# Performance work log

Hardware: AMD Instinct MI355X
Metric: run time of the kernel (lower is better)

## Reference

```python
import jax, jax.numpy as jnp
import numpy as np

EPS = 1e-05

def setup_inputs() -> dict:
    key = jax.random.key(0)
    k1, k2, k3, k4 = jax.random.split(key, 4)
    B, S, D, K = 32, 1024, 768, 16
    x = jax.random.normal(k1, (B, S, D), dtype=jnp.float32)
    # torch init is ones/zeros, but use nontrivial values for a meaningful check
    weights = jax.random.uniform(k2, (K, D), dtype=jnp.float32)
    biases = jax.random.normal(k3, (K, D), dtype=jnp.float32)
    centroids = jax.random.normal(k4, (K, D), dtype=jnp.float32)
    return {"x": x, "weights": weights, "biases": biases, "centroids": centroids}

def reference(x, weights, biases, centroids):
    # LayerNorm over last dim
    mean = jnp.mean(x, axis=-1, keepdims=True)
    diff = x - mean
    var = jnp.mean(jnp.square(diff), axis=-1, keepdims=True)
    normalized = diff / jnp.sqrt(var + EPS)
    # bucket routing: argmin_k ||x - c_k||_2 ; argmin of squared dist is identical
    x2 = jnp.sum(jnp.square(x), axis=-1, keepdims=True)            # [B,S,1]
    c2 = jnp.sum(jnp.square(centroids), axis=-1)                   # [K]
    xc = jnp.einsum("bsd,kd->bsk", x, centroids)                   # [B,S,K]
    sq_dists = x2 - 2.0 * xc + c2
    selected_buckets = jnp.argmin(sq_dists, axis=-1)               # [B,S] int
    # per-position affine via gather of per-bucket weight/bias
    w = weights[selected_buckets]                                  # [B,S,D]
    b = biases[selected_buckets]                                   # [B,S,D]
    out = normalized * w + b
    return (out, selected_buckets)
```

## Files before the change

### kernel.cpp

```cpp
#include <hip/hip_runtime.h>
#include <math.h>

#define DD 768
#define DD4 192
#define KK 16
#define EPSV 1e-5f
#define SCRS 38

__global__ __launch_bounds__(256, 2)
void sln_kernel(const float* __restrict__ x,
                const float* __restrict__ weights,
                const float* __restrict__ biases,
                const float* __restrict__ centroids,
                float* __restrict__ out,
                float* __restrict__ bkt,
                int nrows)
{
    __shared__ float cs[KK * DD];
    __shared__ float c2s[KK];
    __shared__ float scr[4][16][SCRS];

    const int tid  = threadIdx.x;
    const int lane = tid & 63;
    const int wave = tid >> 6;

    {
        const float4* c4 = (const float4*)centroids;
        float4* cs4w = (float4*)cs;
        for (int i = tid; i < KK * DD4; i += 256) cs4w[i] = c4[i];
    }
    __syncthreads();

    {
        float* part = &scr[0][0][0];
        int k = tid >> 4, t = tid & 15;
        float p = 0.f;
        #pragma unroll
        for (int j = 0; j < DD / 16; ++j) {
            float v = cs[k * DD + t + 16 * j];
            p += v * v;
        }
        part[tid] = p;
    }
    __syncthreads();
    if (tid < KK) {
        float* part = &scr[0][0][0];
        float sacc = 0.f;
        #pragma unroll
        for (int i = 0; i < 16; ++i) sacc += part[tid * 16 + i];
        c2s[tid] = sacc;
    }
    __syncthreads();

    const float4* cs4 = (const float4*)cs;
    const int gw = blockIdx.x * 4 + wave;
    const int wstride = gridDim.x * 4;

    for (int pair = gw; pair * 2 < nrows; pair += wstride) {
        const int r0 = pair * 2;
        const int r1 = r0 + 1;

        const float4* xr0 = (const float4*)(x + (size_t)r0 * DD);
        const float4* xr1 = (const float4*)(x + (size_t)r1 * DD);
        float4 a0 = xr0[lane], a1 = xr0[lane + 64], a2 = xr0[lane + 128];
        float4 b0 = xr1[lane], b1 = xr1[lane + 64], b2 = xr1[lane + 128];

        float s0 = a0.x+a0.y+a0.z+a0.w + a1.x+a1.y+a1.z+a1.w + a2.x+a2.y+a2.z+a2.w;
        float ss0 = a0.x*a0.x+a0.y*a0.y+a0.z*a0.z+a0.w*a0.w
                  + a1.x*a1.x+a1.y*a1.y+a1.z*a1.z+a1.w*a1.w
                  + a2.x*a2.x+a2.y*a2.y+a2.z*a2.z+a2.w*a2.w;
        float s1 = b0.x+b0.y+b0.z+b0.w + b1.x+b1.y+b1.z+b1.w + b2.x+b2.y+b2.z+b2.w;
        float ss1 = b0.x*b0.x+b0.y*b0.y+b0.z*b0.z+b0.w*b0.w
                  + b1.x*b1.x+b1.y*b1.y+b1.z*b1.z+b1.w*b1.w
                  + b2.x*b2.x+b2.y*b2.y+b2.z*b2.z+b2.w*b2.w;

        float d0[KK], d1[KK];
        #pragma unroll
        for (int k = 0; k < KK; ++k) {
            float4 c0 = cs4[k * DD4 + lane];
            float4 c1 = cs4[k * DD4 + lane + 64];
            float4 c2 = cs4[k * DD4 + lane + 128];
            d0[k] = a0.x*c0.x + a0.y*c0.y + a0.z*c0.z + a0.w*c0.w
                  + a1.x*c1.x + a1.y*c1.y + a1.z*c1.z + a1.w*c1.w
                  + a2.x*c2.x + a2.y*c2.y + a2.z*c2.z + a2.w*c2.w;
            d1[k] = b0.x*c0.x + b0.y*c0.y + b0.z*c0.z + b0.w*c0.w
                  + b1.x*c1.x + b1.y*c1.y + b1.z*c1.z + b1.w*c1.w
                  + b2.x*c2.x + b2.y*c2.y + b2.z*c2.z + b2.w*c2.w;
        }

        #pragma unroll
        for (int k = 0; k < KK; ++k) {
            d0[k] += __shfl_xor(d0[k], 1); d0[k] += __shfl_xor(d0[k], 2);
            d1[k] += __shfl_xor(d1[k], 1); d1[k] += __shfl_xor(d1[k], 2);
        }
        s0 += __shfl_xor(s0, 1);  s0 += __shfl_xor(s0, 2);
        ss0 += __shfl_xor(ss0, 1); ss0 += __shfl_xor(ss0, 2);
        s1 += __shfl_xor(s1, 1);  s1 += __shfl_xor(s1, 2);
        ss1 += __shfl_xor(ss1, 1); ss1 += __shfl_xor(ss1, 2);

        if ((lane & 3) == 0) {
            int q = lane >> 2;
            float* p = &scr[wave][q][0];
            #pragma unroll
            for (int k = 0; k < KK; ++k) { p[k] = d0[k]; p[18 + k] = d1[k]; }
            p[16] = s0; p[17] = ss0; p[34] = s1; p[35] = ss1;
        }
        __asm__ volatile("" ::: "memory");

        int slot = (lane < 32) ? lane : (18 + (lane - 32));
        float T = 0.f;
        if (lane < 18 || (lane >= 32 && lane < 50)) {
            float t0 = 0.f, t1 = 0.f, t2 = 0.f, t3 = 0.f;
            #pragma unroll
            for (int q = 0; q < 16; q += 4) {
                t0 += scr[wave][q + 0][slot];
                t1 += scr[wave][q + 1][slot];
                t2 += scr[wave][q + 2][slot];
                t3 += scr[wave][q + 3][slot];
            }
            T = (t0 + t1) + (t2 + t3);
        }
        __asm__ volatile("" ::: "memory");

        float sA  = __shfl(T, 16), ssA = __shfl(T, 17);
        float sB  = __shfl(T, 48), ssB = __shfl(T, 49);

        int v = lane & 15;
        float ssSel = (lane & 32) ? ssB : ssA;
        float sq = (ssSel - 2.f * T) + c2s[v];
        int idx = v;
        #pragma unroll
        for (int m = 1; m < 16; m <<= 1) {
            float osq = __shfl_xor(sq, m);
            int   oidx = __shfl_xor(idx, m);
            bool take = (osq < sq) || (osq == sq && oidx < idx);
            sq  = take ? osq  : sq;
            idx = take ? oidx : idx;
        }
        int bk0 = __builtin_amdgcn_readlane(idx, 0);
        int bk1 = __builtin_amdgcn_readlane(idx, 32);

        float mean0 = sA * (1.f / DD);
        float mean1 = sB * (1.f / DD);
        float rstd0 = 1.f / sqrtf(ssA * (1.f / DD) - mean0 * mean0 + EPSV);
        float rstd1 = 1.f / sqrtf(ssB * (1.f / DD) - mean1 * mean1 + EPSV);

        if (lane == 0) {
            bkt[r0] = (float)bk0;
            bkt[r1] = (float)bk1;
        }

        const float4* w0 = (const float4*)(weights + (size_t)bk0 * DD);
        const float4* g0 = (const float4*)(biases  + (size_t)bk0 * DD);
        const float4* w1 = (const float4*)(weights + (size_t)bk1 * DD);
        const float4* g1 = (const float4*)(biases  + (size_t)bk1 * DD);
        float4* o0 = (float4*)(out + (size_t)r0 * DD);
        float4* o1 = (float4*)(out + (size_t)r1 * DD);

        #pragma unroll
        for (int j = 0; j < 3; ++j) {
            float4 xv = (j == 0) ? a0 : (j == 1) ? a1 : a2;
            float4 wv = w0[lane + 64 * j];
            float4 bv = g0[lane + 64 * j];
            float4 o;
            o.x = (xv.x - mean0) * rstd0 * wv.x + bv.x;
            o.y = (xv.y - mean0) * rstd0 * wv.y + bv.y;
            o.z = (xv.z - mean0) * rstd0 * wv.z + bv.z;
            o.w = (xv.w - mean0) * rstd0 * wv.w + bv.w;
            o0[lane + 64 * j] = o;
        }
        #pragma unroll
        for (int j = 0; j < 3; ++j) {
            float4 xv = (j == 0) ? b0 : (j == 1) ? b1 : b2;
            float4 wv = w1[lane + 64 * j];
            float4 bv = g1[lane + 64 * j];
            float4 o;
            o.x = (xv.x - mean1) * rstd1 * wv.x + bv.x;
            o.y = (xv.y - mean1) * rstd1 * wv.y + bv.y;
            o.z = (xv.z - mean1) * rstd1 * wv.z + bv.z;
            o.w = (xv.w - mean1) * rstd1 * wv.w + bv.w;
            o1[lane + 64 * j] = o;
        }
    }
}

extern "C" void kernel_launch(void* const* d_in, const int* in_sizes, int n_in,
                              void* d_out, int out_size, void* d_ws, size_t ws_size,
                              hipStream_t stream) {
    const float* x         = (const float*)d_in[0];
    const float* weights   = (const float*)d_in[1];
    const float* biases    = (const float*)d_in[2];
    const float* centroids = (const float*)d_in[3];

    const int nrows = in_sizes[0] / DD;

    float* out = (float*)d_out;
    float* bkt = out + (size_t)nrows * DD;

    dim3 grid(2048), block(256);
    hipLaunchKernelGGL(sln_kernel, grid, block, 0, stream,
                       x, weights, biases, centroids, out, bkt, nrows);
}
```

Baseline: 198.2 us.

## Prefetch next row pair, use DPP reductions, and retune occupancy and grid

Result: slower. 252.8 us (+27.5%).

```diff
diff --git a/kernel.cpp b/kernel.cpp
--- a/kernel.cpp
+++ b/kernel.cpp
@@ -5,9 +5,24 @@
 #define DD4 192
 #define KK 16
 #define EPSV 1e-5f
-#define SCRS 38
-
-__global__ __launch_bounds__(256, 2)
+
+template <int CTRL>
+__device__ __forceinline__ float dpp_add(float v) {
+    int t = __builtin_amdgcn_update_dpp(0, __float_as_int(v), CTRL, 0xF, 0xF, true);
+    return v + __int_as_float(t);
+}
+#define DPP_XOR1 0xB1
+#define DPP_XOR2 0x4E
+#define DPP_HMIR 0x141
+
+__device__ __forceinline__ float red8(float v) {
+    v = dpp_add<DPP_XOR1>(v);
+    v = dpp_add<DPP_XOR2>(v);
+    v = dpp_add<DPP_HMIR>(v);
+    return v;
+}
+
+__global__ __launch_bounds__(256, 3)
 void sln_kernel(const float* __restrict__ x,
                 const float* __restrict__ weights,
                 const float* __restrict__ biases,
@@ -17,8 +32,7 @@
                 int nrows)
 {
     __shared__ float cs[KK * DD];
-    __shared__ float c2s[KK];
-    __shared__ float scr[4][16][SCRS];
+    __shared__ float scr[4][8][40];
 
     const int tid  = threadIdx.x;
     const int lane = tid & 63;
@@ -31,8 +45,8 @@
     }
     __syncthreads();
 
+    float* flat = &scr[0][0][0];
     {
-        float* part = &scr[0][0][0];
         int k = tid >> 4, t = tid & 15;
         float p = 0.f;
         #pragma unroll
@@ -40,30 +54,45 @@
             float v = cs[k * DD + t + 16 * j];
             p += v * v;
         }
-        part[tid] = p;
+        flat[tid] = p;
     }
     __syncthreads();
     if (tid < KK) {
-        float* part = &scr[0][0][0];
         float sacc = 0.f;
         #pragma unroll
-        for (int i = 0; i < 16; ++i) sacc += part[tid * 16 + i];
-        c2s[tid] = sacc;
-    }
+        for (int i = 0; i < 16; ++i) sacc += flat[tid * 16 + i];
+        flat[256 + tid] = sacc;
+    }
+    __syncthreads();
+    const float c2reg = flat[256 + (lane & 15)];
     __syncthreads();
 
     const float4* cs4 = (const float4*)cs;
-    const int gw = blockIdx.x * 4 + wave;
-    const int wstride = gridDim.x * 4;
-
-    for (int pair = gw; pair * 2 < nrows; pair += wstride) {
-        const int r0 = pair * 2;
-        const int r1 = r0 + 1;
-
-        const float4* xr0 = (const float4*)(x + (size_t)r0 * DD);
-        const float4* xr1 = (const float4*)(x + (size_t)r1 * DD);
-        float4 a0 = xr0[lane], a1 = xr0[lane + 64], a2 = xr0[lane + 128];
-        float4 b0 = xr1[lane], b1 = xr1[lane + 64], b2 = xr1[lane + 128];
+    const int npairs = nrows >> 1;
+    const int pstride = gridDim.x * 4;
+    int pair = blockIdx.x * 4 + wave;
+    bool valid = pair < npairs;
+
+    float4 a0, a1, a2, b0, b1, b2;
+    if (valid) {
+        const float4* xr0 = (const float4*)(x + (size_t)(2 * pair) * DD);
+        const float4* xr1 = (const float4*)(x + (size_t)(2 * pair + 1) * DD);
+        a0 = xr0[lane]; a1 = xr0[lane + 64]; a2 = xr0[lane + 128];
+        b0 = xr1[lane]; b1 = xr1[lane + 64]; b2 = xr1[lane + 128];
+    }
+
+    while (valid) {
+        const int r0 = 2 * pair, r1 = r0 + 1;
+        const int npair = pair + pstride;
+        const bool nvalid = npair < npairs;
+
+        float4 na0, na1, na2, nb0, nb1, nb2;
+        if (nvalid) {
+            const float4* xr0 = (const float4*)(x + (size_t)(2 * npair) * DD);
+            const float4* xr1 = (const float4*)(x + (size_t)(2 * npair + 1) * DD);
+            na0 = xr0[lane]; na1 = xr0[lane + 64]; na2 = xr0[lane + 128];
+            nb0 = xr1[lane]; nb1 = xr1[lane + 64]; nb2 = xr1[lane + 128];
+        }
 
         float s0 = a0.x+a0.y+a0.z+a0.w + a1.x+a1.y+a1.z+a1.w + a2.x+a2.y+a2.z+a2.w;
         float ss0 = a0.x*a0.x+a0.y*a0.y+a0.z*a0.z+a0.w*a0.w
@@ -89,45 +118,44 @@
         }
 
         #pragma unroll
-        for (int k = 0; k < KK; ++k) {
-            d0[k] += __shfl_xor(d0[k], 1); d0[k] += __shfl_xor(d0[k], 2);
-            d1[k] += __shfl_xor(d1[k], 1); d1[k] += __shfl_xor(d1[k], 2);
-        }
-        s0 += __shfl_xor(s0, 1);  s0 += __shfl_xor(s0, 2);
-        ss0 += __shfl_xor(ss0, 1); ss0 += __shfl_xor(ss0, 2);
-        s1 += __shfl_xor(s1, 1);  s1 += __shfl_xor(s1, 2);
-        ss1 += __shfl_xor(ss1, 1); ss1 += __shfl_xor(ss1, 2);
-
-        if ((lane & 3) == 0) {
-            int q = lane >> 2;
-            float* p = &scr[wave][q][0];
-            #pragma unroll
-            for (int k = 0; k < KK; ++k) { p[k] = d0[k]; p[18 + k] = d1[k]; }
-            p[16] = s0; p[17] = ss0; p[34] = s1; p[35] = ss1;
+        for (int k = 0; k < KK; ++k) { d0[k] = red8(d0[k]); d1[k] = red8(d1[k]); }
+        s0 = red8(s0); ss0 = red8(ss0); s1 = red8(s1); ss1 = red8(ss1);
+
+        if ((lane & 7) == 0) {
+            int g = lane >> 3;
+            float4* p4 = (float4*)&scr[wave][g][0];
+            p4[0] = make_float4(d0[0],  d0[1],  d0[2],  d0[3]);
+            p4[1] = make_float4(d0[4],  d0[5],  d0[6],  d0[7]);
+            p4[2] = make_float4(d0[8],  d0[9],  d0[10], d0[11]);
+            p4[3] = make_float4(d0[12], d0[13], d0[14], d0[15]);
+            p4[4] = make_float4(s0, ss0, d1[0], d1[1]);
+            p4[5] = make_float4(d1[2],  d1[3],  d1[4],  d1[5]);
+            p4[6] = make_float4(d1[6],  d1[7],  d1[8],  d1[9]);
+            p4[7] = make_float4(d1[10], d1[11], d1[12], d1[13]);
+            p4[8] = make_float4(d1[14], d1[15], s1, ss1);
         }
         __asm__ volatile("" ::: "memory");
 
-        int slot = (lane < 32) ? lane : (18 + (lane - 32));
         float T = 0.f;
         if (lane < 18 || (lane >= 32 && lane < 50)) {
+            int slot = (lane < 32) ? lane : (lane - 14);
             float t0 = 0.f, t1 = 0.f, t2 = 0.f, t3 = 0.f;
-            #pragma unroll
-            for (int q = 0; q < 16; q += 4) {
-                t0 += scr[wave][q + 0][slot];
-                t1 += scr[wave][q + 1][slot];
-                t2 += scr[wave][q + 2][slot];
-                t3 += scr[wave][q + 3][slot];
-            }
+            t0 = scr[wave][0][slot] + scr[wave][4][slot];
+            t1 = scr[wave][1][slot] + scr[wave][5][slot];
+            t2 = scr[wave][2][slot] + scr[wave][6][slot];
+            t3 = scr[wave][3][slot] + scr[wave][7][slot];
             T = (t0 + t1) + (t2 + t3);
         }
         __asm__ volatile("" ::: "memory");
 
-        float sA  = __shfl(T, 16), ssA = __shfl(T, 17);
-        float sB  = __shfl(T, 48), ssB = __shfl(T, 49);
-
-        int v = lane & 15;
-        float ssSel = (lane & 32) ? ssB : ssA;
-        float sq = (ssSel - 2.f * T) + c2s[v];
+        const float sA  = __int_as_float(__builtin_amdgcn_readlane(__float_as_int(T), 16));
+        const float ssA = __int_as_float(__builtin_amdgcn_readlane(__float_as_int(T), 17));
+        const float sB  = __int_as_float(__builtin_amdgcn_readlane(__float_as_int(T), 48));
+        const float ssB = __int_as_float(__builtin_amdgcn_readlane(__float_as_int(T), 49));
+
+        const int v = lane & 15;
+        const float ssSel = (lane & 32) ? ssB : ssA;
+        float sq = (ssSel - 2.f * T) + c2reg;
         int idx = v;
         #pragma unroll
         for (int m = 1; m < 16; m <<= 1) {
@@ -137,13 +165,13 @@
             sq  = take ? osq  : sq;
             idx = take ? oidx : idx;
         }
-        int bk0 = __builtin_amdgcn_readlane(idx, 0);
-        int bk1 = __builtin_amdgcn_readlane(idx, 32);
-
-        float mean0 = sA * (1.f / DD);
-        float mean1 = sB * (1.f / DD);
-        float rstd0 = 1.f / sqrtf(ssA * (1.f / DD) - mean0 * mean0 + EPSV);
-        float rstd1 = 1.f / sqrtf(ssB * (1.f / DD) - mean1 * mean1 + EPSV);
+        const int bk0 = __builtin_amdgcn_readlane(idx, 0);
+        const int bk1 = __builtin_amdgcn_readlane(idx, 32);
+
+        const float mean0 = sA * (1.f / DD);
+        const float mean1 = sB * (1.f / DD);
+        const float rstd0 = 1.f / sqrtf(ssA * (1.f / DD) - mean0 * mean0 + EPSV);
+        const float rstd1 = 1.f / sqrtf(ssB * (1.f / DD) - mean1 * mean1 + EPSV);
 
         if (lane == 0) {
             bkt[r0] = (float)bk0;
@@ -181,6 +209,10 @@
             o.w = (xv.w - mean1) * rstd1 * wv.w + bv.w;
             o1[lane + 64 * j] = o;
         }
+
+        a0 = na0; a1 = na1; a2 = na2;
+        b0 = nb0; b1 = nb1; b2 = nb2;
+        pair = npair; valid = nvalid;
     }
 }
 
@@ -197,7 +229,7 @@
     float* out = (float*)d_out;
     float* bkt = out + (size_t)nrows * DD;
 
-    dim3 grid(2048), block(256);
+    dim3 grid(768), block(256);
     hipLaunchKernelGGL(sln_kernel, grid, block, 0, stream,
                        x, weights, biases, centroids, out, bkt, nrows);
 }
```
